# Performance work log

Hardware: AMD Instinct MI355X
Metric: run time of the kernel (lower is better)

The kernel has to match this reference:

```python
import jax, jax.numpy as jnp
import numpy as np

HEAD = 8
DIM_HEAD = 64
EPS = 1e-5  # torch GroupNorm default


def group_norm(x, w, b, groups, eps=EPS):
    # x: [B, C, H, W]; normalize per (group, spatial)
    B, C, H, W = x.shape
    xg = x.reshape(B, groups, C // groups, H, W)
    mu = xg.mean(axis=(2, 3, 4), keepdims=True)
    var = xg.var(axis=(2, 3, 4), keepdims=True)
    xn = ((xg - mu) / jnp.sqrt(var + eps)).reshape(B, C, H, W)
    return xn * w[None, :, None, None] + b[None, :, None, None]


def setup_inputs() -> dict:
    key = jax.random.key(0)
    ks = jax.random.split(key, 4)
    dim = 256
    hidden = HEAD * DIM_HEAD  # 512
    x = jax.random.normal(ks[0], (16, dim, 64, 64), dtype=jnp.float32)
    qkv_w = jax.random.normal(ks[1], (hidden * 3, dim), dtype=jnp.float32) * 0.02
    out_w = jax.random.normal(ks[2], (dim, hidden), dtype=jnp.float32) * 0.02
    out_b = jnp.zeros((dim,), dtype=jnp.float32)
    gn1_w = jnp.ones((dim,), dtype=jnp.float32)
    gn1_b = jnp.zeros((dim,), dtype=jnp.float32)
    gn2_w = jnp.ones((dim,), dtype=jnp.float32)
    gn2_b = jnp.zeros((dim,), dtype=jnp.float32)
    return {"x": x, "gn1_w": gn1_w, "gn1_b": gn1_b, "qkv_w": qkv_w,
            "out_w": out_w, "out_b": out_b, "gn2_w": gn2_w, "gn2_b": gn2_b}


def reference(x, gn1_w, gn1_b, qkv_w, out_w, out_b, gn2_w, gn2_b):
    B, C, I, J = x.shape
    groups = C // 8
    scale = DIM_HEAD ** -0.5
    n = I * J

    xn = group_norm(x, gn1_w, gn1_b, groups)
    # 1x1 conv == channel matmul: [B,3*hidden,I,J]
    qkv = jnp.einsum('bchw,oc->bohw', xn, qkv_w)
    q, k, v = jnp.split(qkv, 3, axis=1)

    def to_heads(t):  # [B, h*f, I, J] -> [B, h, f, n]
        return t.reshape(B, HEAD, DIM_HEAD, n)

    q = jax.nn.softmax(to_heads(q), axis=-2) * scale  # softmax over feature dim
    k = jax.nn.softmax(to_heads(k), axis=-1)          # softmax over spatial dim
    v = to_heads(v)

    context = jnp.einsum('bhfm,bhem->bhfe', k, v)     # [B,h,f,e]
    attn = jnp.einsum('bhfe,bhfn->bhen', context, q)  # [B,h,e,n]
    out = attn.reshape(B, HEAD * DIM_HEAD, I, J)

    out = jnp.einsum('bchw,oc->bohw', out, out_w) + out_b[None, :, None, None]
    return group_norm(out, gn2_w, gn2_b, groups)
```

## Files before the change

### kernel.cpp

```cpp
#include <hip/hip_runtime.h>
#include <math.h>

#define NB   16
#define NC   256
#define NP   4096
#define NHD  8
#define FD   64
#define HID  512
#define OC3  1536
#define NG   32
#define CPG  8
#define GEPS 1e-5f

typedef __attribute__((ext_vector_type(8))) short bf16x8;
typedef __attribute__((ext_vector_type(4))) float f32x4;

#define MFMA_BF16(a, b, c) __builtin_amdgcn_mfma_f32_16x16x32_bf16(a, b, c, 0, 0, 0)

__device__ __forceinline__ uint bf16_rne(float v) {
    uint u = __float_as_uint(v);
    return (u + 0x7FFFu + ((u >> 16) & 1u)) >> 16;
}
__device__ __forceinline__ void split2(float v, uint& h, uint& l) {
    h = bf16_rne(v);
    l = bf16_rne(v - __uint_as_float(h << 16));
}
__device__ __forceinline__ void gload16(const void* g, void* l) {
    __builtin_amdgcn_global_load_lds(
        (const __attribute__((address_space(1))) void*)g,
        (__attribute__((address_space(3))) void*)l, 16, 0, 0);
}

__global__ __launch_bounds__(256) void gn_stats_kernel(const float* __restrict__ x,
                                                       float* __restrict__ mu,
                                                       float* __restrict__ rstd) {
    int bg = blockIdx.x;
    const float4* b4 = (const float4*)(x + (size_t)bg * CPG * NP);
    int t = threadIdx.x;
    float s = 0.f, sq = 0.f;
    #pragma unroll
    for (int i = 0; i < 32; ++i) {
        float4 v = b4[t + i * 256];
        s  += v.x + v.y + v.z + v.w;
        sq += v.x*v.x + v.y*v.y + v.z*v.z + v.w*v.w;
    }
    for (int off = 32; off; off >>= 1) { s += __shfl_down(s, off); sq += __shfl_down(sq, off); }
    __shared__ float ss[4], ssq[4];
    int wid = t >> 6, lane = t & 63;
    if (lane == 0) { ss[wid] = s; ssq[wid] = sq; }
    __syncthreads();
    if (t == 0) {
        float S  = ss[0] + ss[1] + ss[2] + ss[3];
        float SQ = ssq[0] + ssq[1] + ssq[2] + ssq[3];
        const float inv = 1.f / (float)(CPG * NP);
        float m = S * inv;
        float var = SQ * inv - m * m;
        mu[bg] = m;
        rstd[bg] = rsqrtf(var + GEPS);
    }
}

__global__ void gn1_coefs_kernel(const float* __restrict__ mu, const float* __restrict__ rstd,
                                 const float* __restrict__ w, const float* __restrict__ bias,
                                 float* __restrict__ ac, float* __restrict__ dc) {
    int i = blockIdx.x * 256 + threadIdx.x;
    if (i >= NB * NC) return;
    int b = i / NC, c = i % NC;
    int g = c / CPG;
    float m = mu[b * NG + g], r = rstd[b * NG + g];
    float a = r * w[c];
    ac[i] = a;
    dc[i] = bias[c] - m * a;
}

__global__ void wsplit_kernel(const float* __restrict__ w, ushort* __restrict__ wh,
                              ushort* __restrict__ wl) {
    int i = blockIdx.x * 256 + threadIdx.x;
    float4 v = ((const float4*)w)[i];
    uint h, l;
    ushort4 hv, lv;
    split2(v.x, h, l); hv.x = (ushort)h; lv.x = (ushort)l;
    split2(v.y, h, l); hv.y = (ushort)h; lv.y = (ushort)l;
    split2(v.z, h, l); hv.z = (ushort)h; lv.z = (ushort)l;
    split2(v.w, h, l); hv.w = (ushort)h; lv.w = (ushort)l;
    ((ushort4*)wh)[i] = hv;
    ((ushort4*)wl)[i] = lv;
}

__global__ __launch_bounds__(256) void xsplit_kernel(const float* __restrict__ x,
                                                     const float* __restrict__ ac,
                                                     const float* __restrict__ dc,
                                                     ushort* __restrict__ xTh,
                                                     ushort* __restrict__ xTl, int b0) {
    int z = blockIdx.z, bglob = b0 + z;
    int p0 = blockIdx.x * 64, c0 = blockIdx.y * 64;
    const float* xb = x + (size_t)bglob * NC * NP;
    __shared__ float T[64][72];
    int t = threadIdx.x;
    #pragma unroll
    for (int j = 0; j < 4; ++j) {
        int idx = t + j * 256;
        int r = idx >> 4, c4 = idx & 15;
        float4 v = *(const float4*)(xb + (size_t)(c0 + r) * NP + p0 + c4 * 4);
        float a = ac[bglob * NC + c0 + r], d = dc[bglob * NC + c0 + r];
        v.x = fmaf(v.x, a, d); v.y = fmaf(v.y, a, d);
        v.z = fmaf(v.z, a, d); v.w = fmaf(v.w, a, d);
        *(float4*)&T[r][c4 * 4] = v;
    }
    __syncthreads();
    int p = t >> 2, cseg = t & 3;
    size_t ob = ((size_t)z * NP + p0 + p) * NC + c0 + cseg * 16;
    #pragma unroll
    for (int half = 0; half < 2; ++half) {
        uint4 uh, ul;
        uint* ph = (uint*)&uh; uint* pl = (uint*)&ul;
        #pragma unroll
        for (int i = 0; i < 4; ++i) {
            int c = cseg * 16 + half * 8 + i * 2;
            uint h0, l0, h1, l1;
            split2(T[c][p], h0, l0);
            split2(T[c + 1][p], h1, l1);
            ph[i] = h0 | (h1 << 16);
            pl[i] = l0 | (l1 << 16);
        }
        *(uint4*)(xTh + ob + half * 8) = uh;
        *(uint4*)(xTl + ob + half * 8) = ul;
    }
}

__global__ __launch_bounds__(256) void gemm_q_kernel(
        const ushort* __restrict__ Ah, const ushort* __restrict__ Al,
        const ushort* __restrict__ Bhg, const ushort* __restrict__ Blg,
        ushort* __restrict__ qsTh, ushort* __restrict__ qsTl) {
    __shared__ __align__(16) char smem[33280];
    const int z = blockIdx.z;
    const ushort* Bh = Bhg + (size_t)NP * NC * z;
    const ushort* Bl = Blg + (size_t)NP * NC * z;

    const int t = threadIdx.x;
    const int w = t >> 6, l = t & 63;
    const int wr = w >> 1, wc = w & 1;
    const int m0 = blockIdx.y * 128, n0 = blockIdx.x * 128;
    const int l15 = l & 15, kb = l >> 4;

    f32x4 acc[4][4];
    #pragma unroll
    for (int i = 0; i < 4; ++i)
        #pragma unroll
        for (int j = 0; j < 4; ++j)
            acc[i][j] = (f32x4){0.f, 0.f, 0.f, 0.f};

    for (int k0 = 0; k0 < NC; k0 += 32) {
        #pragma unroll
        for (int j = 0; j < 2; ++j) {
            int idx = t + j * 256;
            int m = idx & 127, s = idx >> 7;
            size_t goA = (size_t)(m0 + m) * NC + k0 + s * 8;
            size_t goB = (size_t)(n0 + m) * NC + k0 + s * 8;
            int lo = idx * 16;
            gload16(Ah + goA, smem + lo);
            gload16(Al + goA, smem + 8192 + lo);
            gload16(Bh + goB, smem + 16384 + lo);
            gload16(Bl + goB, smem + 24576 + lo);
        }
        __syncthreads();
        bf16x8 ah[4], al[4];
        #pragma unroll
        for (int fi = 0; fi < 4; ++fi) {
            int off = (kb * 128 + wr * 64 + fi * 16 + l15) * 16;
            ah[fi] = *(const bf16x8*)(smem + off);
            al[fi] = *(const bf16x8*)(smem + 8192 + off);
        }
        #pragma unroll
        for (int fj = 0; fj < 4; ++fj) {
            int off = (kb * 128 + wc * 64 + fj * 16 + l15) * 16;
            bf16x8 bh = *(const bf16x8*)(smem + 16384 + off);
            bf16x8 bl = *(const bf16x8*)(smem + 24576 + off);
            #pragma unroll
            for (int fi = 0; fi < 4; ++fi) {
                acc[fi][fj] = MFMA_BF16(ah[fi], bh, acc[fi][fj]);
                acc[fi][fj] = MFMA_BF16(al[fi], bh, acc[fi][fj]);
                acc[fi][fj] = MFMA_BF16(ah[fi], bl, acc[fi][fj]);
            }
        }
        __syncthreads();
    }

    uint* Tq = (uint*)smem;
    #pragma unroll
    for (int half = 0; half < 2; ++half) {
        if (wc == half) {
            #pragma unroll
            for (int fj = 0; fj < 4; ++fj) {
                float ex[16];
                float cs = 0.f;
                #pragma unroll
                for (int fi = 0; fi < 4; ++fi)
                    #pragma unroll
                    for (int r = 0; r < 4; ++r) {
                        float e = __expf(acc[fi][fj][r]);
                        ex[fi * 4 + r] = e;
                        cs += e;
                    }
                cs += __shfl_xor(cs, 16);
                cs += __shfl_xor(cs, 32);
                float inv = 0.125f / cs;
                int p_loc = fj * 16 + l15;
                #pragma unroll
                for (int fi = 0; fi < 4; ++fi)
                    #pragma unroll
                    for (int r = 0; r < 4; ++r) {
                        uint hb, lb;
                        split2(ex[fi * 4 + r] * inv, hb, lb);
                        Tq[p_loc * 130 + wr * 64 + fi * 16 + kb * 4 + r] = (hb << 16) | lb;
                    }
            }
        }
        __syncthreads();
        int p = t >> 2, seg = t & 3;
        size_t ob = ((size_t)z * NP + n0 + half * 64 + p) * HID + m0 + seg * 32;
        #pragma unroll
        for (int c = 0; c < 4; ++c) {
            uint4 H, L;
            uint* hp = (uint*)&H; uint* lp = (uint*)&L;
            #pragma unroll
            for (int i = 0; i < 4; ++i) {
                uint u0 = Tq[p * 130 + seg * 32 + c * 8 + 2 * i];
                uint u1 = Tq[p * 130 + seg * 32 + c * 8 + 2 * i + 1];
                hp[i] = (u0 >> 16) | (u1 & 0xffff0000u);
                lp[i] = (u0 & 0xffffu) | (u1 << 16);
            }
            *(uint4*)(qsTh + ob + c * 8) = H;
            *(uint4*)(qsTl + ob + c * 8) = L;
        }
        __syncthreads();
    }
}

__global__ __launch_bounds__(512, 4) void kv_ctx_kernel(
        const ushort* __restrict__ Wh, const ushort* __restrict__ Wl,
        const ushort* __restrict__ Bhg, const ushort* __restrict__ Blg,
        float* __restrict__ ctxp, float* __restrict__ kspart) {
    __shared__ __align__(16) char smem[69632];
    const int z = blockIdx.z;
    const int h = blockIdx.y;
    const int tile = blockIdx.x;
    const int n0 = tile * 128;
    const ushort* Bh = Bhg + (size_t)NP * NC * z;
    const ushort* Bl = Blg + (size_t)NP * NC * z;

    const int t = threadIdx.x;
    const int w = t >> 6, l = t & 63;
    const int wr = w >> 2, wc = w & 3;
    const int l15 = l & 15, kb = l >> 4;

    ushort* ekh = (ushort*)smem;
    ushort* ekl = ekh + 64 * 136;
    ushort* vh_ = ekl + 64 * 136;
    ushort* vl_ = vh_ + 64 * 136;

    f32x4 acc[4][2];
    #pragma unroll
    for (int i = 0; i < 4; ++i)
        #pragma unroll
        for (int j = 0; j < 2; ++j)
            acc[i][j] = (f32x4){0.f, 0.f, 0.f, 0.f};

    for (int k0 = 0; k0 < NC; k0 += 32) {
        {
            int idx = t;
            int m = idx & 127, s = idx >> 7;
            int grow = 512 + h * 64 + (m & 63) + ((m >> 6) << 9);
            size_t goA = (size_t)grow * NC + k0 + s * 8;
            size_t goB = (size_t)(n0 + m) * NC + k0 + s * 8;
            int lo = idx * 16;
            gload16(Wh + goA, smem + lo);
            gload16(Wl + goA, smem + 8192 + lo);
            gload16(Bh + goB, smem + 16384 + lo);
            gload16(Bl + goB, smem + 24576 + lo);
        }
        __syncthreads();
        bf16x8 ah[4], al[4];
        #pragma unroll
        for (int fi = 0; fi < 4; ++fi) {
            int off = (kb * 128 + wr * 64 + fi * 16 + l15) * 16;
            ah[fi] = *(const bf16x8*)(smem + off);
            al[fi] = *(const bf16x8*)(smem + 8192 + off);
        }
        #pragma unroll
        for (int fj = 0; fj < 2; ++fj) {
            int off = (kb * 128 + wc * 32 + fj * 16 + l15) * 16;
            bf16x8 bh = *(const bf16x8*)(smem + 16384 + off);
            bf16x8 bl = *(const bf16x8*)(smem + 24576 + off);
            #pragma unroll
            for (int fi = 0; fi < 4; ++fi) {
                acc[fi][fj] = MFMA_BF16(ah[fi], bh, acc[fi][fj]);
                acc[fi][fj] = MFMA_BF16(al[fi], bh, acc[fi][fj]);
                acc[fi][fj] = MFMA_BF16(ah[fi], bl, acc[fi][fj]);
            }
        }
        __syncthreads();
    }

    #pragma unroll
    for (int fi = 0; fi < 4; ++fi) {
        #pragma unroll
        for (int r = 0; r < 4; ++r) {
            int row = fi * 16 + kb * 4 + r;
            float rs = 0.f;
            #pragma unroll
            for (int fj = 0; fj < 2; ++fj) {
                float v = acc[fi][fj][r];
                float e = (wr == 0) ? __expf(v) : v;
                rs += e;
                uint hb, lb;
                split2(e, hb, lb);
                int P = wc * 32 + fj * 16 + l15;
                if (wr == 0) { ekh[row * 136 + P] = (ushort)hb; ekl[row * 136 + P] = (ushort)lb; }
                else         { vh_[row * 136 + P] = (ushort)hb; vl_[row * 136 + P] = (ushort)lb; }
            }
            if (wr == 0) {
                rs += __shfl_xor(rs, 1); rs += __shfl_xor(rs, 2);
                rs += __shfl_xor(rs, 4); rs += __shfl_xor(rs, 8);
                if (l15 == 0)
                    kspart[((size_t)z * HID + h * 64 + row) * 128 + tile * 4 + wc] = rs;
            }
        }
    }
    __syncthreads();

    f32x4 c2[2];
    c2[0] = (f32x4){0.f, 0.f, 0.f, 0.f};
    c2[1] = (f32x4){0.f, 0.f, 0.f, 0.f};
    const int cr0 = (w >> 2) * 32;
    const int cc0 = (w & 3) * 16;
    #pragma unroll
    for (int ks = 0; ks < 4; ++ks) {
        bf16x8 a_h[2], a_l[2];
        #pragma unroll
        for (int i = 0; i < 2; ++i) {
            int offa = (cr0 + i * 16 + l15) * 136 + ks * 32 + kb * 8;
            a_h[i] = *(const bf16x8*)(ekh + offa);
            a_l[i] = *(const bf16x8*)(ekl + offa);
        }
        int offb = (cc0 + l15) * 136 + ks * 32 + kb * 8;
        bf16x8 b_h = *(const bf16x8*)(vh_ + offb);
        bf16x8 b_l = *(const bf16x8*)(vl_ + offb);
        #pragma unroll
        for (int i = 0; i < 2; ++i) {
            c2[i] = MFMA_BF16(a_h[i], b_h, c2[i]);
            c2[i] = MFMA_BF16(a_l[i], b_h, c2[i]);
            c2[i] = MFMA_BF16(a_h[i], b_l, c2[i]);
        }
    }
    float* outp = ctxp + (((size_t)z * NHD + h) * 32 + tile) * 4096;
    #pragma unroll
    for (int i = 0; i < 2; ++i)
        #pragma unroll
        for (int r = 0; r < 4; ++r)
            outp[(size_t)(cr0 + i * 16 + kb * 4 + r) * 64 + cc0 + l15] = c2[i][r];
}

__global__ void ksum_reduce_kernel(const float* __restrict__ kspart,
                                   float* __restrict__ ksum, int n) {
    int i = blockIdx.x * 256 + threadIdx.x;
    if (i >= n) return;
    float s = 0.f;
    #pragma unroll
    for (int j = 0; j < 128; ++j) s += kspart[(size_t)i * 128 + j];
    ksum[i] = s;
}

__global__ void ctx_reduce_kernel(const float* __restrict__ ctxp, float* __restrict__ ctx,
                                  int n4) {
    int i = blockIdx.x * 256 + threadIdx.x;
    if (i >= n4) return;
    int zh = i >> 10, i4 = i & 1023;
    const float4* p = (const float4*)ctxp + (size_t)zh * 32 * 1024;
    float4 r = {0.f, 0.f, 0.f, 0.f};
    #pragma unroll
    for (int s = 0; s < 32; ++s) {
        float4 a = p[(size_t)s * 1024 + i4];
        r.x += a.x; r.y += a.y; r.z += a.z; r.w += a.w;
    }
    ((float4*)ctx)[(size_t)zh * 1024 + i4] = r;
}

__global__ __launch_bounds__(256) void fold_kernel(const float* __restrict__ out_w,
                                                   const float* __restrict__ ctx,
                                                   const float* __restrict__ ksum,
                                                   ushort* __restrict__ w2h,
                                                   ushort* __restrict__ w2l) {
    int h = blockIdx.x, z = blockIdx.y;
    __shared__ float Cs[FD][FD];
    int t = threadIdx.x;
    const float* cbase = ctx + ((size_t)z * NHD + h) * FD * FD;
    #pragma unroll
    for (int j = 0; j < 16; ++j) ((float*)Cs)[t + j * 256] = cbase[t + j * 256];
    __syncthreads();
    float wr[64];
    const float* wrow = out_w + (size_t)t * HID + h * FD;
    #pragma unroll
    for (int e = 0; e < 64; ++e) wr[e] = wrow[e];
    size_t ob = ((size_t)z * NC + t) * HID + h * FD;
    for (int f = 0; f < 64; ++f) {
        float sacc = 0.f;
        #pragma unroll
        for (int e = 0; e < 64; ++e) sacc = fmaf(wr[e], Cs[f][e], sacc);
        float v = sacc / ksum[(size_t)z * HID + h * FD + f];
        uint hb, lb;
        split2(v, hb, lb);
        w2h[ob + f] = (ushort)hb;
        w2l[ob + f] = (ushort)lb;
    }
}

__global__ __launch_bounds__(256) void gemm_out_kernel(
        const ushort* __restrict__ Ahg, const ushort* __restrict__ Alg,
        const ushort* __restrict__ Bhg, const ushort* __restrict__ Blg,
        const float* __restrict__ bias, float* __restrict__ outg,
        float2* __restrict__ gn2part, int b0) {
    __shared__ __align__(16) char smem[32768];
    const int z = blockIdx.z, bglob = b0 + z;
    const ushort* Ah = Ahg + (size_t)NC * HID * z;
    const ushort* Al = Alg + (size_t)NC * HID * z;
    const ushort* Bh = Bhg + (size_t)NP * HID * z;
    const ushort* Bl = Blg + (size_t)NP * HID * z;
    float* C = outg + (size_t)bglob * NC * NP;

    const int t = threadIdx.x;
    const int w = t >> 6, l = t & 63;
    const int wr = w >> 1, wc = w & 1;
    const int m0 = blockIdx.y * 128, n0 = blockIdx.x * 128;
    const int l15 = l & 15, kb = l >> 4;

    f32x4 acc[4][4];
    #pragma unroll
    for (int i = 0; i < 4; ++i)
        #pragma unroll
        for (int j = 0; j < 4; ++j)
            acc[i][j] = (f32x4){0.f, 0.f, 0.f, 0.f};

    for (int k0 = 0; k0 < HID; k0 += 32) {
        #pragma unroll
        for (int j = 0; j < 2; ++j) {
            int idx = t + j * 256;
            int m = idx & 127, s = idx >> 7;
            size_t goA = (size_t)(m0 + m) * HID + k0 + s * 8;
            size_t goB = (size_t)(n0 + m) * HID + k0 + s * 8;
            int lo = idx * 16;
            gload16(Ah + goA, smem + lo);
            gload16(Al + goA, smem + 8192 + lo);
            gload16(Bh + goB, smem + 16384 + lo);
            gload16(Bl + goB, smem + 24576 + lo);
        }
        __syncthreads();
        bf16x8 ah[4], al[4];
        #pragma unroll
        for (int fi = 0; fi < 4; ++fi) {
            int off = (kb * 128 + wr * 64 + fi * 16 + l15) * 16;
            ah[fi] = *(const bf16x8*)(smem + off);
            al[fi] = *(const bf16x8*)(smem + 8192 + off);
        }
        #pragma unroll
        for (int fj = 0; fj < 4; ++fj) {
            int off = (kb * 128 + wc * 64 + fj * 16 + l15) * 16;
            bf16x8 bh = *(const bf16x8*)(smem + 16384 + off);
            bf16x8 bl = *(const bf16x8*)(smem + 24576 + off);
            #pragma unroll
            for (int fi = 0; fi < 4; ++fi) {
                acc[fi][fj] = MFMA_BF16(ah[fi], bh, acc[fi][fj]);
                acc[fi][fj] = MFMA_BF16(al[fi], bh, acc[fi][fj]);
                acc[fi][fj] = MFMA_BF16(ah[fi], bl, acc[fi][fj]);
            }
        }
        __syncthreads();
    }

    float gs[4] = {0.f, 0.f, 0.f, 0.f}, gq[4] = {0.f, 0.f, 0.f, 0.f};
    #pragma unroll
    for (int fi = 0; fi < 4; ++fi) {
        int mbase = m0 + wr * 64 + fi * 16 + kb * 4;
        #pragma unroll
        for (int fj = 0; fj < 4; ++fj) {
            int n = n0 + wc * 64 + fj * 16 + l15;
            #pragma unroll
            for (int r = 0; r < 4; ++r) {
                float v = acc[fi][fj][r] + bias[mbase + r];
                C[(size_t)(mbase + r) * NP + n] = v;
                gs[fi] += v;
                gq[fi] += v * v;
            }
        }
    }
    #pragma unroll
    for (int fi = 0; fi < 4; ++fi) {
        #pragma unroll
        for (int d = 1; d <= 16; d <<= 1) {
            gs[fi] += __shfl_xor(gs[fi], d);
            gq[fi] += __shfl_xor(gq[fi], d);
        }
    }
    if (l15 == 0 && (kb & 1) == 0) {
        #pragma unroll
        for (int fi = 0; fi < 4; ++fi) {
            int g = ((m0 + wr * 64) >> 3) + fi * 2 + (kb >> 1);
            float2 pv; pv.x = gs[fi]; pv.y = gq[fi];
            gn2part[(((size_t)bglob * NG + g) << 6) + blockIdx.x * 2 + wc] = pv;
        }
    }
}

__global__ void gn2_reduce_kernel(const float2* __restrict__ gn2part,
                                  float* __restrict__ mu, float* __restrict__ rstd) {
    int i = blockIdx.x * 256 + threadIdx.x;
    if (i >= NB * NG) return;
    float s = 0.f, q = 0.f;
    #pragma unroll
    for (int j = 0; j < 64; ++j) {
        float2 p = gn2part[((size_t)i << 6) + j];
        s += p.x; q += p.y;
    }
    const float inv = 1.f / (float)(CPG * NP);
    float m = s * inv;
    float var = q * inv - m * m;
    mu[i] = m;
    rstd[i] = rsqrtf(var + GEPS);
}

__global__ void gn2_apply_kernel(float* __restrict__ out, const float* __restrict__ mu,
                                 const float* __restrict__ rstd, const float* __restrict__ w,
                                 const float* __restrict__ bias) {
    int i = blockIdx.x * 256 + threadIdx.x;
    float4* p = (float4*)out;
    float4 v = p[i];
    size_t e0 = (size_t)i * 4;
    int cidx = (int)((e0 / NP) % NC);
    int bg   = (int)(e0 / ((size_t)CPG * NP));
    float m = mu[bg], r = rstd[bg];
    float a = r * w[cidx];
    float d = bias[cidx] - m * a;
    v.x = fmaf(v.x, a, d); v.y = fmaf(v.y, a, d);
    v.z = fmaf(v.z, a, d); v.w = fmaf(v.w, a, d);
    p[i] = v;
}

extern "C" void kernel_launch(void* const* d_in, const int* in_sizes, int n_in,
                              void* d_out, int out_size, void* d_ws, size_t ws_size,
                              hipStream_t stream) {
    const float* x     = (const float*)d_in[0];
    const float* gn1_w = (const float*)d_in[1];
    const float* gn1_b = (const float*)d_in[2];
    const float* qkv_w = (const float*)d_in[3];
    const float* out_w = (const float*)d_in[4];
    const float* out_b = (const float*)d_in[5];
    const float* gn2_w = (const float*)d_in[6];
    const float* gn2_b = (const float*)d_in[7];
    float* out = (float*)d_out;

    auto need = [](int cb) -> size_t {
        size_t tot = 0;
        auto al = [&](size_t b) { tot = (tot + b + 255) & ~(size_t)255; };
        al((size_t)cb * NP * NC * 2);  al((size_t)cb * NP * NC * 2);
        al((size_t)cb * NP * HID * 2); al((size_t)cb * NP * HID * 2);
        al((size_t)cb * NHD * 32 * FD * FD * 4);
        al((size_t)cb * NHD * FD * FD * 4);
        al((size_t)cb * HID * 128 * 4);
        al((size_t)cb * HID * 4);
        al((size_t)cb * NC * HID * 2); al((size_t)cb * NC * HID * 2);
        al((size_t)OC3 * NC * 2); al((size_t)OC3 * NC * 2);
        al((size_t)2 * NB * NC * 4);
        al((size_t)4 * NB * NG * 4);
        al((size_t)NB * NG * 64 * 8);
        return tot;
    };
    int CB = 1;
    {
        const int cands[5] = {16, 8, 4, 2, 1};
        for (int i = 0; i < 5; ++i) if (need(cands[i]) <= ws_size) { CB = cands[i]; break; }
    }

    char* base = (char*)d_ws;
    size_t off = 0;
    auto carve = [&](size_t b) -> char* {
        char* p = base + off;
        off = (off + b + 255) & ~(size_t)255;
        return p;
    };
    ushort* xTh  = (ushort*)carve((size_t)CB * NP * NC * 2);
    ushort* xTl  = (ushort*)carve((size_t)CB * NP * NC * 2);
    ushort* qsTh = (ushort*)carve((size_t)CB * NP * HID * 2);
    ushort* qsTl = (ushort*)carve((size_t)CB * NP * HID * 2);
    float*  ctxp = (float*) carve((size_t)CB * NHD * 32 * FD * FD * 4);
    float*  ctx  = (float*) carve((size_t)CB * NHD * FD * FD * 4);
    float*  kspart = (float*)carve((size_t)CB * HID * 128 * 4);
    float*  ksum = (float*) carve((size_t)CB * HID * 4);
    ushort* w2h  = (ushort*)carve((size_t)CB * NC * HID * 2);
    ushort* w2l  = (ushort*)carve((size_t)CB * NC * HID * 2);
    ushort* Wqh  = (ushort*)carve((size_t)OC3 * NC * 2);
    ushort* Wql  = (ushort*)carve((size_t)OC3 * NC * 2);
    float*  ac   = (float*) carve((size_t)2 * NB * NC * 4);
    float*  dc   = ac + (size_t)NB * NC;
    float*  mu1  = (float*) carve((size_t)4 * NB * NG * 4);
    float*  rstd1 = mu1 + NB * NG;
    float*  mu2   = rstd1 + NB * NG;
    float*  rstd2 = mu2 + NB * NG;
    float2* gn2part = (float2*)carve((size_t)NB * NG * 64 * 8);

    gn_stats_kernel<<<NB * NG, 256, 0, stream>>>(x, mu1, rstd1);
    gn1_coefs_kernel<<<16, 256, 0, stream>>>(mu1, rstd1, gn1_w, gn1_b, ac, dc);
    wsplit_kernel<<<OC3 * NC / 1024, 256, 0, stream>>>(qkv_w, Wqh, Wql);

    for (int b0 = 0; b0 < NB; b0 += CB) {
        xsplit_kernel<<<dim3(NP / 64, NC / 64, CB), 256, 0, stream>>>(x, ac, dc, xTh, xTl, b0);
        gemm_q_kernel<<<dim3(NP / 128, 4, CB), 256, 0, stream>>>(Wqh, Wql, xTh, xTl, qsTh, qsTl);
        kv_ctx_kernel<<<dim3(NP / 128, NHD, CB), 512, 0, stream>>>(Wqh, Wql, xTh, xTl, ctxp, kspart);
        ksum_reduce_kernel<<<(CB * HID + 255) / 256, 256, 0, stream>>>(kspart, ksum, CB * HID);
        ctx_reduce_kernel<<<CB * 32, 256, 0, stream>>>(ctxp, ctx, CB * NHD * 1024);
        fold_kernel<<<dim3(NHD, CB), 256, 0, stream>>>(out_w, ctx, ksum, w2h, w2l);
        gemm_out_kernel<<<dim3(NP / 128, 2, CB), 256, 0, stream>>>(
            w2h, w2l, qsTh, qsTl, out_b, out, gn2part, b0);
    }

    gn2_reduce_kernel<<<2, 256, 0, stream>>>(gn2part, mu2, rstd2);
    gn2_apply_kernel<<<16384, 256, 0, stream>>>(out, mu2, rstd2, gn2_w, gn2_b);
}
```

Baseline: 564.9 us.

## Accumulate context over four tiles per block and fold reduction into fold_kernel

```diff
diff --git a/kernel.cpp b/kernel.cpp
--- a/kernel.cpp
+++ b/kernel.cpp
@@ -244,8 +244,7 @@
     __shared__ __align__(16) char smem[69632];
     const int z = blockIdx.z;
     const int h = blockIdx.y;
-    const int tile = blockIdx.x;
-    const int n0 = tile * 128;
+    const int tg = blockIdx.x;
     const ushort* Bh = Bhg + (size_t)NP * NC * z;
     const ushort* Bl = Blg + (size_t)NP * NC * z;
 
@@ -258,102 +257,110 @@
     ushort* ekl = ekh + 64 * 136;
     ushort* vh_ = ekl + 64 * 136;
     ushort* vl_ = vh_ + 64 * 136;
-
-    f32x4 acc[4][2];
-    #pragma unroll
-    for (int i = 0; i < 4; ++i)
-        #pragma unroll
-        for (int j = 0; j < 2; ++j)
-            acc[i][j] = (f32x4){0.f, 0.f, 0.f, 0.f};
-
-    for (int k0 = 0; k0 < NC; k0 += 32) {
-        {
-            int idx = t;
-            int m = idx & 127, s = idx >> 7;
-            int grow = 512 + h * 64 + (m & 63) + ((m >> 6) << 9);
-            size_t goA = (size_t)grow * NC + k0 + s * 8;
-            size_t goB = (size_t)(n0 + m) * NC + k0 + s * 8;
-            int lo = idx * 16;
-            gload16(Wh + goA, smem + lo);
-            gload16(Wl + goA, smem + 8192 + lo);
-            gload16(Bh + goB, smem + 16384 + lo);
-            gload16(Bl + goB, smem + 24576 + lo);
-        }
-        __syncthreads();
-        bf16x8 ah[4], al[4];
-        #pragma unroll
-        for (int fi = 0; fi < 4; ++fi) {
-            int off = (kb * 128 + wr * 64 + fi * 16 + l15) * 16;
-            ah[fi] = *(const bf16x8*)(smem + off);
-            al[fi] = *(const bf16x8*)(smem + 8192 + off);
-        }
-        #pragma unroll
-        for (int fj = 0; fj < 2; ++fj) {
-            int off = (kb * 128 + wc * 32 + fj * 16 + l15) * 16;
-            bf16x8 bh = *(const bf16x8*)(smem + 16384 + off);
-            bf16x8 bl = *(const bf16x8*)(smem + 24576 + off);
-            #pragma unroll
-            for (int fi = 0; fi < 4; ++fi) {
-                acc[fi][fj] = MFMA_BF16(ah[fi], bh, acc[fi][fj]);
-                acc[fi][fj] = MFMA_BF16(al[fi], bh, acc[fi][fj]);
-                acc[fi][fj] = MFMA_BF16(ah[fi], bl, acc[fi][fj]);
-            }
-        }
-        __syncthreads();
-    }
-
-    #pragma unroll
-    for (int fi = 0; fi < 4; ++fi) {
-        #pragma unroll
-        for (int r = 0; r < 4; ++r) {
-            int row = fi * 16 + kb * 4 + r;
-            float rs = 0.f;
-            #pragma unroll
-            for (int fj = 0; fj < 2; ++fj) {
-                float v = acc[fi][fj][r];
-                float e = (wr == 0) ? __expf(v) : v;
-                rs += e;
-                uint hb, lb;
-                split2(e, hb, lb);
-                int P = wc * 32 + fj * 16 + l15;
-                if (wr == 0) { ekh[row * 136 + P] = (ushort)hb; ekl[row * 136 + P] = (ushort)lb; }
-                else         { vh_[row * 136 + P] = (ushort)hb; vl_[row * 136 + P] = (ushort)lb; }
-            }
-            if (wr == 0) {
-                rs += __shfl_xor(rs, 1); rs += __shfl_xor(rs, 2);
-                rs += __shfl_xor(rs, 4); rs += __shfl_xor(rs, 8);
-                if (l15 == 0)
-                    kspart[((size_t)z * HID + h * 64 + row) * 128 + tile * 4 + wc] = rs;
-            }
-        }
-    }
-    __syncthreads();
 
     f32x4 c2[2];
     c2[0] = (f32x4){0.f, 0.f, 0.f, 0.f};
     c2[1] = (f32x4){0.f, 0.f, 0.f, 0.f};
     const int cr0 = (w >> 2) * 32;
     const int cc0 = (w & 3) * 16;
-    #pragma unroll
-    for (int ks = 0; ks < 4; ++ks) {
-        bf16x8 a_h[2], a_l[2];
-        #pragma unroll
-        for (int i = 0; i < 2; ++i) {
-            int offa = (cr0 + i * 16 + l15) * 136 + ks * 32 + kb * 8;
-            a_h[i] = *(const bf16x8*)(ekh + offa);
-            a_l[i] = *(const bf16x8*)(ekl + offa);
-        }
-        int offb = (cc0 + l15) * 136 + ks * 32 + kb * 8;
-        bf16x8 b_h = *(const bf16x8*)(vh_ + offb);
-        bf16x8 b_l = *(const bf16x8*)(vl_ + offb);
-        #pragma unroll
-        for (int i = 0; i < 2; ++i) {
-            c2[i] = MFMA_BF16(a_h[i], b_h, c2[i]);
-            c2[i] = MFMA_BF16(a_l[i], b_h, c2[i]);
-            c2[i] = MFMA_BF16(a_h[i], b_l, c2[i]);
-        }
-    }
-    float* outp = ctxp + (((size_t)z * NHD + h) * 32 + tile) * 4096;
+
+    for (int it = 0; it < 4; ++it) {
+        const int tile = tg * 4 + it;
+        const int n0 = tile * 128;
+        __syncthreads();
+
+        f32x4 acc[4][2];
+        #pragma unroll
+        for (int i = 0; i < 4; ++i)
+            #pragma unroll
+            for (int j = 0; j < 2; ++j)
+                acc[i][j] = (f32x4){0.f, 0.f, 0.f, 0.f};
+
+        for (int k0 = 0; k0 < NC; k0 += 32) {
+            {
+                int idx = t;
+                int m = idx & 127, s = idx >> 7;
+                int grow = 512 + h * 64 + (m & 63) + ((m >> 6) << 9);
+                size_t goA = (size_t)grow * NC + k0 + s * 8;
+                size_t goB = (size_t)(n0 + m) * NC + k0 + s * 8;
+                int lo = idx * 16;
+                gload16(Wh + goA, smem + lo);
+                gload16(Wl + goA, smem + 8192 + lo);
+                gload16(Bh + goB, smem + 16384 + lo);
+                gload16(Bl + goB, smem + 24576 + lo);
+            }
+            __syncthreads();
+            bf16x8 ah[4], al[4];
+            #pragma unroll
+            for (int fi = 0; fi < 4; ++fi) {
+                int off = (kb * 128 + wr * 64 + fi * 16 + l15) * 16;
+                ah[fi] = *(const bf16x8*)(smem + off);
+                al[fi] = *(const bf16x8*)(smem + 8192 + off);
+            }
+            #pragma unroll
+            for (int fj = 0; fj < 2; ++fj) {
+                int off = (kb * 128 + wc * 32 + fj * 16 + l15) * 16;
+                bf16x8 bh = *(const bf16x8*)(smem + 16384 + off);
+                bf16x8 bl = *(const bf16x8*)(smem + 24576 + off);
+                #pragma unroll
+                for (int fi = 0; fi < 4; ++fi) {
+                    acc[fi][fj] = MFMA_BF16(ah[fi], bh, acc[fi][fj]);
+                    acc[fi][fj] = MFMA_BF16(al[fi], bh, acc[fi][fj]);
+                    acc[fi][fj] = MFMA_BF16(ah[fi], bl, acc[fi][fj]);
+                }
+            }
+            __syncthreads();
+        }
+
+        #pragma unroll
+        for (int fi = 0; fi < 4; ++fi) {
+            #pragma unroll
+            for (int r = 0; r < 4; ++r) {
+                int row = fi * 16 + kb * 4 + r;
+                float rs = 0.f;
+                #pragma unroll
+                for (int fj = 0; fj < 2; ++fj) {
+                    float v = acc[fi][fj][r];
+                    float e = (wr == 0) ? __expf(v) : v;
+                    rs += e;
+                    uint hb, lb;
+                    split2(e, hb, lb);
+                    int P = wc * 32 + fj * 16 + l15;
+                    if (wr == 0) { ekh[row * 136 + P] = (ushort)hb; ekl[row * 136 + P] = (ushort)lb; }
+                    else         { vh_[row * 136 + P] = (ushort)hb; vl_[row * 136 + P] = (ushort)lb; }
+                }
+                if (wr == 0) {
+                    rs += __shfl_xor(rs, 1); rs += __shfl_xor(rs, 2);
+                    rs += __shfl_xor(rs, 4); rs += __shfl_xor(rs, 8);
+                    if (l15 == 0)
+                        kspart[((size_t)z * HID + h * 64 + row) * 128 + tile * 4 + wc] = rs;
+                }
+            }
+        }
+        __syncthreads();
+
+        #pragma unroll
+        for (int ks = 0; ks < 4; ++ks) {
+            bf16x8 a_h[2], a_l[2];
+            #pragma unroll
+            for (int i = 0; i < 2; ++i) {
+                int offa = (cr0 + i * 16 + l15) * 136 + ks * 32 + kb * 8;
+                a_h[i] = *(const bf16x8*)(ekh + offa);
+                a_l[i] = *(const bf16x8*)(ekl + offa);
+            }
+            int offb = (cc0 + l15) * 136 + ks * 32 + kb * 8;
+            bf16x8 b_h = *(const bf16x8*)(vh_ + offb);
+            bf16x8 b_l = *(const bf16x8*)(vl_ + offb);
+            #pragma unroll
+            for (int i = 0; i < 2; ++i) {
+                c2[i] = MFMA_BF16(a_h[i], b_h, c2[i]);
+                c2[i] = MFMA_BF16(a_l[i], b_h, c2[i]);
+                c2[i] = MFMA_BF16(a_h[i], b_l, c2[i]);
+            }
+        }
+    }
+
+    float* outp = ctxp + (((size_t)z * NHD + h) * 8 + tg) * 4096;
     #pragma unroll
     for (int i = 0; i < 2; ++i)
         #pragma unroll
@@ -371,32 +378,23 @@
     ksum[i] = s;
 }
 
-__global__ void ctx_reduce_kernel(const float* __restrict__ ctxp, float* __restrict__ ctx,
-                                  int n4) {
-    int i = blockIdx.x * 256 + threadIdx.x;
-    if (i >= n4) return;
-    int zh = i >> 10, i4 = i & 1023;
-    const float4* p = (const float4*)ctxp + (size_t)zh * 32 * 1024;
-    float4 r = {0.f, 0.f, 0.f, 0.f};
-    #pragma unroll
-    for (int s = 0; s < 32; ++s) {
-        float4 a = p[(size_t)s * 1024 + i4];
-        r.x += a.x; r.y += a.y; r.z += a.z; r.w += a.w;
-    }
-    ((float4*)ctx)[(size_t)zh * 1024 + i4] = r;
-}
-
 __global__ __launch_bounds__(256) void fold_kernel(const float* __restrict__ out_w,
-                                                   const float* __restrict__ ctx,
+                                                   const float* __restrict__ ctxp,
                                                    const float* __restrict__ ksum,
                                                    ushort* __restrict__ w2h,
                                                    ushort* __restrict__ w2l) {
     int h = blockIdx.x, z = blockIdx.y;
     __shared__ float Cs[FD][FD];
     int t = threadIdx.x;
-    const float* cbase = ctx + ((size_t)z * NHD + h) * FD * FD;
-    #pragma unroll
-    for (int j = 0; j < 16; ++j) ((float*)Cs)[t + j * 256] = cbase[t + j * 256];
+    const float* pbase = ctxp + ((size_t)z * NHD + h) * 8 * 4096;
+    #pragma unroll
+    for (int j = 0; j < 16; ++j) {
+        int idx = t + j * 256;
+        float s = 0.f;
+        #pragma unroll
+        for (int p8 = 0; p8 < 8; ++p8) s += pbase[(size_t)p8 * 4096 + idx];
+        ((float*)Cs)[idx] = s;
+    }
     __syncthreads();
     float wr[64];
     const float* wrow = out_w + (size_t)t * HID + h * FD;
@@ -563,8 +561,7 @@
         auto al = [&](size_t b) { tot = (tot + b + 255) & ~(size_t)255; };
         al((size_t)cb * NP * NC * 2);  al((size_t)cb * NP * NC * 2);
         al((size_t)cb * NP * HID * 2); al((size_t)cb * NP * HID * 2);
-        al((size_t)cb * NHD * 32 * FD * FD * 4);
-        al((size_t)cb * NHD * FD * FD * 4);
+        al((size_t)cb * NHD * 8 * FD * FD * 4);
         al((size_t)cb * HID * 128 * 4);
         al((size_t)cb * HID * 4);
         al((size_t)cb * NC * HID * 2); al((size_t)cb * NC * HID * 2);
@@ -591,8 +588,7 @@
     ushort* xTl  = (ushort*)carve((size_t)CB * NP * NC * 2);
     ushort* qsTh = (ushort*)carve((size_t)CB * NP * HID * 2);
     ushort* qsTl = (ushort*)carve((size_t)CB * NP * HID * 2);
-    float*  ctxp = (float*) carve((size_t)CB * NHD * 32 * FD * FD * 4);
-    float*  ctx  = (float*) carve((size_t)CB * NHD * FD * FD * 4);
+    float*  ctxp = (float*) carve((size_t)CB * NHD * 8 * FD * FD * 4);
     float*  kspart = (float*)carve((size_t)CB * HID * 128 * 4);
     float*  ksum = (float*) carve((size_t)CB * HID * 4);
     ushort* w2h  = (ushort*)carve((size_t)CB * NC * HID * 2);
@@ -613,11 +609,10 @@
 
     for (int b0 = 0; b0 < NB; b0 += CB) {
         xsplit_kernel<<<dim3(NP / 64, NC / 64, CB), 256, 0, stream>>>(x, ac, dc, xTh, xTl, b0);
+        kv_ctx_kernel<<<dim3(8, NHD, CB), 512, 0, stream>>>(Wqh, Wql, xTh, xTl, ctxp, kspart);
+        ksum_reduce_kernel<<<(CB * HID + 255) / 256, 256, 0, stream>>>(kspart, ksum, CB * HID);
         gemm_q_kernel<<<dim3(NP / 128, 4, CB), 256, 0, stream>>>(Wqh, Wql, xTh, xTl, qsTh, qsTl);
-        kv_ctx_kernel<<<dim3(NP / 128, NHD, CB), 512, 0, stream>>>(Wqh, Wql, xTh, xTl, ctxp, kspart);
-        ksum_reduce_kernel<<<(CB * HID + 255) / 256, 256, 0, stream>>>(kspart, ksum, CB * HID);
-        ctx_reduce_kernel<<<CB * 32, 256, 0, stream>>>(ctxp, ctx, CB * NHD * 1024);
-        fold_kernel<<<dim3(NHD, CB), 256, 0, stream>>>(out_w, ctx, ksum, w2h, w2l);
+        fold_kernel<<<dim3(NHD, CB), 256, 0, stream>>>(out_w, ctxp, ksum, w2h, w2l);
         gemm_out_kernel<<<dim3(NP / 128, 2, CB), 256, 0, stream>>>(
             w2h, w2l, qsTh, qsTl, out_b, out, gn2part, b0);
     }
```

Result: faster. 546.3 us (-3.3%).
